# Kernel optimization log

Measured on AMD Instinct MI355X. Metric: run time of the kernel, lower is better.

## Reference

```python
import jax, jax.numpy as jnp
import numpy as np

GROUPS = 16
GROUP_SIZE = 16
K = 3
KK = K * K
BN_EPS = 1e-5


def setup_inputs() -> dict:
    key = jax.random.key(0)
    ks = jax.random.split(key, 6)
    B, C, H, W = 16, 256, 56, 56
    mid = C // 4  # rd_ratio = 4
    x = jax.random.normal(ks[0], (B, C, H, W), dtype=jnp.float32)
    w1 = jax.random.normal(ks[1], (mid, C), dtype=jnp.float32) * (1.0 / np.sqrt(C))
    bn_gamma = jnp.ones((mid,), dtype=jnp.float32)
    bn_beta = jnp.zeros((mid,), dtype=jnp.float32)
    bn_mean = jax.random.normal(ks[2], (mid,), dtype=jnp.float32) * 0.1
    bn_var = jax.random.uniform(ks[3], (mid,), dtype=jnp.float32, minval=0.5, maxval=1.5)
    w2 = jax.random.normal(ks[4], (KK * GROUPS, mid), dtype=jnp.float32) * (1.0 / np.sqrt(mid))
    b2 = jax.random.normal(ks[5], (KK * GROUPS,), dtype=jnp.float32) * 0.01
    return {"x": x, "w1": w1, "bn_gamma": bn_gamma, "bn_beta": bn_beta,
            "bn_mean": bn_mean, "bn_var": bn_var, "w2": w2, "b2": b2}


def reference(x, w1, bn_gamma, bn_beta, bn_mean, bn_var, w2, b2):
    B, C, H, W = x.shape
    # conv1: 1x1 conv + BatchNorm (eval) + ReLU
    t = jnp.einsum('bchw,oc->bohw', x, w1)
    scale = bn_gamma / jnp.sqrt(bn_var + BN_EPS)
    t = t * scale[None, :, None, None] + (bn_beta - bn_mean * scale)[None, :, None, None]
    t = jax.nn.relu(t)
    # conv2: 1x1 conv producing per-pixel kernels (B, KK*groups, H, W)
    weight = jnp.einsum('bchw,oc->bohw', t, w2) + b2[None, :, None, None]
    weight = weight.reshape(B, GROUPS, 1, KK, H, W)
    # unfold: extract 3x3 patches (pad=1, stride=1), kernel positions row-major
    xp = jnp.pad(x, ((0, 0), (0, 0), (1, 1), (1, 1)))
    patches = jnp.stack(
        [xp[:, :, i:i + H, j:j + W] for i in range(K) for j in range(K)],
        axis=2)  # (B, C, KK, H, W), matches torch unfold's (c*KK + kk) layout
    patches = patches.reshape(B, GROUPS, GROUP_SIZE, KK, H, W)
    out = (weight * patches).sum(axis=3).reshape(B, C, H, W)
    return out
```

## Files before the change

### kernel.cpp

```cpp
#include <hip/hip_runtime.h>


#define Cn    256
#define MID   64
#define Hn    56
#define Wn    56
#define HW    3136
#define Bn    16
#define NPIX  (Bn * HW)
#define CHW   (Cn * HW)
#define NKK   9
#define NG    16
#define GSZ   16
#define PXT   64
#define BN_EPS 1e-5f

#define GLOAD_LDS(src, dst, sz)                                                        \
  __builtin_amdgcn_global_load_lds(                                                    \
      (const __attribute__((address_space(1))) void*)(src),                            \
      (__attribute__((address_space(3))) void*)(dst), (sz), 0, 0)

__global__ __launch_bounds__(256) void prep_kernel(
    const float* __restrict__ w1,
    const float* __restrict__ gamma,
    const float* __restrict__ beta,
    const float* __restrict__ mean,
    const float* __restrict__ var,
    float* __restrict__ w1f,
    float* __restrict__ bias1) {
  int idx = blockIdx.x * 256 + threadIdx.x;
  if (idx < MID * Cn) {
    int c = idx >> 6;
    int o = idx & 63;
    float scale = gamma[o] / sqrtf(var[o] + BN_EPS);
    w1f[idx] = w1[o * Cn + c] * scale;
  } else if (idx < MID * Cn + MID) {
    int o = idx - MID * Cn;
    float scale = gamma[o] / sqrtf(var[o] + BN_EPS);
    bias1[o] = beta[o] - mean[o] * scale;
  }
}

__global__ __launch_bounds__(256) void conv1_kernel(
    const float* __restrict__ x,
    const float* __restrict__ w1f,
    const float* __restrict__ bias1,
    float* __restrict__ t) {
  __shared__ __align__(16) float sb[4096];

  const int tid = threadIdx.x;
  const int px  = tid & 63;
  const int wvv = tid >> 6;
  const int wv  = __builtin_amdgcn_readfirstlane(wvv);

  const int px0 = blockIdx.x * PXT;
  const int b   = px0 / HW;
  const int hw0 = px0 - b * HW;
  const float* xb = x + (size_t)b * CHW + hw0;

#pragma unroll
  for (int j = 0; j < 4; ++j) {
    const int c = (wv << 2) + j;
    GLOAD_LDS(xb + (size_t)c * HW + px, &sb[c * 64], 4);
  }
  GLOAD_LDS(w1f + (wv << 8) + (px << 2), &sb[2048 + (wv << 8)], 16);
  __syncthreads();

  float acc[16];
#pragma unroll
  for (int j = 0; j < 16; ++j) acc[j] = 0.0f;

  for (int k = 0; k < 16; ++k) {
    const int cur = k & 1;
    if (k < 15) {
      const int nb = cur ^ 1;
      const int kb = k + 1;
#pragma unroll
      for (int j = 0; j < 4; ++j) {
        const int c = (wv << 2) + j;
        GLOAD_LDS(xb + (size_t)(kb * 16 + c) * HW + px, &sb[nb * 1024 + c * 64], 4);
      }
      GLOAD_LDS(w1f + kb * 1024 + (wv << 8) + (px << 2),
                &sb[2048 + nb * 1024 + (wv << 8)], 16);
    }
    const float* lx = &sb[cur * 1024];
    const float* lw = &sb[2048 + cur * 1024 + (wv << 4)];
#pragma unroll
    for (int c = 0; c < 16; ++c) {
      const float xv = lx[(c << 6) + px];
      const float4 w40 = *(const float4*)(lw + (c << 6) + 0);
      const float4 w41 = *(const float4*)(lw + (c << 6) + 4);
      const float4 w42 = *(const float4*)(lw + (c << 6) + 8);
      const float4 w43 = *(const float4*)(lw + (c << 6) + 12);
      acc[0]  = fmaf(xv, w40.x, acc[0]);
      acc[1]  = fmaf(xv, w40.y, acc[1]);
      acc[2]  = fmaf(xv, w40.z, acc[2]);
      acc[3]  = fmaf(xv, w40.w, acc[3]);
      acc[4]  = fmaf(xv, w41.x, acc[4]);
      acc[5]  = fmaf(xv, w41.y, acc[5]);
      acc[6]  = fmaf(xv, w41.z, acc[6]);
      acc[7]  = fmaf(xv, w41.w, acc[7]);
      acc[8]  = fmaf(xv, w42.x, acc[8]);
      acc[9]  = fmaf(xv, w42.y, acc[9]);
      acc[10] = fmaf(xv, w42.z, acc[10]);
      acc[11] = fmaf(xv, w42.w, acc[11]);
      acc[12] = fmaf(xv, w43.x, acc[12]);
      acc[13] = fmaf(xv, w43.y, acc[13]);
      acc[14] = fmaf(xv, w43.z, acc[14]);
      acc[15] = fmaf(xv, w43.w, acc[15]);
    }
    __syncthreads();
  }

#pragma unroll
  for (int j = 0; j < 16; ++j) {
    const int o = (wv << 4) + j;
    t[(size_t)o * NPIX + px0 + px] = fmaxf(acc[j] + bias1[o], 0.0f);
  }
}

__global__ __launch_bounds__(256) void conv2_inv_kernel(
    const float* __restrict__ x,
    const float* __restrict__ t,
    const float* __restrict__ w2,
    const float* __restrict__ b2,
    float* __restrict__ out) {
  __shared__ float lt[MID][PXT];
  __shared__ __align__(16) float lw2f[4 * NKK * MID];

  const int tid = threadIdx.x;
  const int px  = tid & 63;
  const int wvv = tid >> 6;
  const int wv  = __builtin_amdgcn_readfirstlane(wvv);

  const int bid = blockIdx.x;
  const int pc  = bid >> 2;
  const int gq  = bid & 3;
  const int g   = (gq << 2) + wv;

  const int px0 = pc * PXT;
  const int b   = px0 / HW;
  const int hw0 = px0 - b * HW;

#pragma unroll
  for (int j = 0; j < 16; ++j) {
    const int o = (wv << 4) + j;
    GLOAD_LDS(t + (size_t)o * NPIX + px0 + px, &lt[o][0], 4);
  }
  for (int ch = wv; ch < 9; ch += 4) {
    GLOAD_LDS(w2 + (size_t)gq * (4 * NKK * MID) + (ch << 8) + (px << 2),
              &lw2f[ch << 8], 16);
  }
  __syncthreads();

  float a[NKK];
#pragma unroll
  for (int kk = 0; kk < NKK; ++kk) a[kk] = b2[g * NKK + kk];
  const float* wq = &lw2f[wv * (NKK * MID)];
#pragma unroll 4
  for (int o4 = 0; o4 < MID; o4 += 4) {
    const float t0 = lt[o4 + 0][px];
    const float t1 = lt[o4 + 1][px];
    const float t2 = lt[o4 + 2][px];
    const float t3 = lt[o4 + 3][px];
#pragma unroll
    for (int kk = 0; kk < NKK; ++kk) {
      const float4 w4 = *(const float4*)&wq[(kk << 6) + o4];
      a[kk] = fmaf(t3, w4.w, fmaf(t2, w4.z, fmaf(t1, w4.y, fmaf(t0, w4.x, a[kk]))));
    }
  }

  const int hw = hw0 + px;
  const int h  = hw / Wn;
  const int w  = hw - h * Wn;

  int off[NKK];
  unsigned vmask = 0;
#pragma unroll
  for (int kk = 0; kk < NKK; ++kk) {
    const int di  = kk / 3 - 1;
    const int dj  = kk % 3 - 1;
    const int h2  = h + di;
    const int w2v = w + dj;
    const bool valid = ((unsigned)h2 < (unsigned)Hn) && ((unsigned)w2v < (unsigned)Wn);
    off[kk] = valid ? (h2 * Wn + w2v) : hw;
    vmask |= (valid ? 1u : 0u) << kk;
  }

  float wk[NKK];
#pragma unroll
  for (int kk = 0; kk < NKK; ++kk)
    wk[kk] = ((vmask >> kk) & 1u) ? a[kk] : 0.0f;

  const float* xc = x + (size_t)b * CHW + (size_t)(g * GSZ) * HW;
  float* ob = out + (size_t)b * CHW + (size_t)(g * GSZ) * HW + hw;
#pragma unroll 4
  for (int cc = 0; cc < GSZ; ++cc) {
    const float* xp = xc + (size_t)cc * HW;
    float s0 = wk[0] * xp[off[0]];
    float s1 = wk[1] * xp[off[1]];
    float s2 = wk[2] * xp[off[2]];
    s0 = fmaf(wk[3], xp[off[3]], s0);
    s1 = fmaf(wk[4], xp[off[4]], s1);
    s2 = fmaf(wk[5], xp[off[5]], s2);
    s0 = fmaf(wk[6], xp[off[6]], s0);
    s1 = fmaf(wk[7], xp[off[7]], s1);
    s2 = fmaf(wk[8], xp[off[8]], s2);
    ob[(size_t)cc * HW] = s0 + s1 + s2;
  }
}

extern "C" void kernel_launch(void* const* d_in, const int* in_sizes, int n_in,
                              void* d_out, int out_size, void* d_ws, size_t ws_size,
                              hipStream_t stream) {
  const float* x     = (const float*)d_in[0];
  const float* w1    = (const float*)d_in[1];
  const float* gamma = (const float*)d_in[2];
  const float* beta  = (const float*)d_in[3];
  const float* mean  = (const float*)d_in[4];
  const float* var   = (const float*)d_in[5];
  const float* w2    = (const float*)d_in[6];
  const float* b2    = (const float*)d_in[7];
  float* out = (float*)d_out;

  char* ws = (char*)d_ws;
  float* t     = (float*)ws;
  float* w1f   = (float*)(ws + (size_t)MID * NPIX * 4);
  float* bias1 = (float*)(ws + (size_t)MID * NPIX * 4 + (size_t)MID * Cn * 4);

  prep_kernel<<<(MID * Cn + MID + 255) / 256, 256, 0, stream>>>(
      w1, gamma, beta, mean, var, w1f, bias1);
  conv1_kernel<<<NPIX / PXT, 256, 0, stream>>>(x, w1f, bias1, t);
  conv2_inv_kernel<<<NPIX / PXT * 4, 256, 0, stream>>>(x, t, w2, b2, out);
}
```

Baseline: 176.4 us.

## Split conv1 output channels across two blocks and read weights from global memory

conv1 now launches twice as many blocks, each computing 32 of the 64 output channels with 8 accumulators per thread. Weights are read directly from global memory through wave-uniform addresses instead of being staged in LDS. Both kernels now use 16-byte global-to-LDS loads for the activation tiles. The aim is more parallelism, lower register and LDS pressure, and fewer load instructions. The cost is that x is read twice in conv1 and weight loads go through the cache rather than LDS.

Measured after the change: 161.9 us. -8.2%, faster.

```diff
diff --git a/kernel.cpp b/kernel.cpp
--- a/kernel.cpp
+++ b/kernel.cpp
@@ -46,75 +46,57 @@
     const float* __restrict__ w1f,
     const float* __restrict__ bias1,
     float* __restrict__ t) {
-  __shared__ __align__(16) float sb[4096];
+  __shared__ __align__(16) float lx[2][16][PXT];
 
   const int tid = threadIdx.x;
   const int px  = tid & 63;
-  const int wvv = tid >> 6;
-  const int wv  = __builtin_amdgcn_readfirstlane(wvv);
-
-  const int px0 = blockIdx.x * PXT;
+  const int wv  = __builtin_amdgcn_readfirstlane(tid >> 6);
+
+  const int bid = blockIdx.x;
+  const int pc  = bid >> 1;
+  const int oh  = bid & 1;
+  const int px0 = pc * PXT;
   const int b   = px0 / HW;
   const int hw0 = px0 - b * HW;
   const float* xb = x + (size_t)b * CHW + hw0;
 
-#pragma unroll
-  for (int j = 0; j < 4; ++j) {
-    const int c = (wv << 2) + j;
-    GLOAD_LDS(xb + (size_t)c * HW + px, &sb[c * 64], 4);
-  }
-  GLOAD_LDS(w1f + (wv << 8) + (px << 2), &sb[2048 + (wv << 8)], 16);
+  const int rsub = px >> 4;
+  const int csub = (px & 15) << 2;
+
+  GLOAD_LDS(xb + (size_t)((wv << 2) + rsub) * HW + csub, &lx[0][wv << 2][0], 16);
   __syncthreads();
 
-  float acc[16];
-#pragma unroll
-  for (int j = 0; j < 16; ++j) acc[j] = 0.0f;
+  float acc[8];
+#pragma unroll
+  for (int j = 0; j < 8; ++j) acc[j] = 0.0f;
 
   for (int k = 0; k < 16; ++k) {
     const int cur = k & 1;
     if (k < 15) {
-      const int nb = cur ^ 1;
-      const int kb = k + 1;
-#pragma unroll
-      for (int j = 0; j < 4; ++j) {
-        const int c = (wv << 2) + j;
-        GLOAD_LDS(xb + (size_t)(kb * 16 + c) * HW + px, &sb[nb * 1024 + c * 64], 4);
-      }
-      GLOAD_LDS(w1f + kb * 1024 + (wv << 8) + (px << 2),
-                &sb[2048 + nb * 1024 + (wv << 8)], 16);
+      GLOAD_LDS(xb + (size_t)((k + 1) * 16 + (wv << 2) + rsub) * HW + csub,
+                &lx[cur ^ 1][wv << 2][0], 16);
     }
-    const float* lx = &sb[cur * 1024];
-    const float* lw = &sb[2048 + cur * 1024 + (wv << 4)];
 #pragma unroll
     for (int c = 0; c < 16; ++c) {
-      const float xv = lx[(c << 6) + px];
-      const float4 w40 = *(const float4*)(lw + (c << 6) + 0);
-      const float4 w41 = *(const float4*)(lw + (c << 6) + 4);
-      const float4 w42 = *(const float4*)(lw + (c << 6) + 8);
-      const float4 w43 = *(const float4*)(lw + (c << 6) + 12);
-      acc[0]  = fmaf(xv, w40.x, acc[0]);
-      acc[1]  = fmaf(xv, w40.y, acc[1]);
-      acc[2]  = fmaf(xv, w40.z, acc[2]);
-      acc[3]  = fmaf(xv, w40.w, acc[3]);
-      acc[4]  = fmaf(xv, w41.x, acc[4]);
-      acc[5]  = fmaf(xv, w41.y, acc[5]);
-      acc[6]  = fmaf(xv, w41.z, acc[6]);
-      acc[7]  = fmaf(xv, w41.w, acc[7]);
-      acc[8]  = fmaf(xv, w42.x, acc[8]);
-      acc[9]  = fmaf(xv, w42.y, acc[9]);
-      acc[10] = fmaf(xv, w42.z, acc[10]);
-      acc[11] = fmaf(xv, w42.w, acc[11]);
-      acc[12] = fmaf(xv, w43.x, acc[12]);
-      acc[13] = fmaf(xv, w43.y, acc[13]);
-      acc[14] = fmaf(xv, w43.z, acc[14]);
-      acc[15] = fmaf(xv, w43.w, acc[15]);
+      const float xv = lx[cur][c][px];
+      const float* wr = w1f + (((k << 4) + c) << 6) + (oh << 5) + (wv << 3);
+      const float4 wa = *(const float4*)(wr + 0);
+      const float4 wb = *(const float4*)(wr + 4);
+      acc[0] = fmaf(xv, wa.x, acc[0]);
+      acc[1] = fmaf(xv, wa.y, acc[1]);
+      acc[2] = fmaf(xv, wa.z, acc[2]);
+      acc[3] = fmaf(xv, wa.w, acc[3]);
+      acc[4] = fmaf(xv, wb.x, acc[4]);
+      acc[5] = fmaf(xv, wb.y, acc[5]);
+      acc[6] = fmaf(xv, wb.z, acc[6]);
+      acc[7] = fmaf(xv, wb.w, acc[7]);
     }
     __syncthreads();
   }
 
 #pragma unroll
-  for (int j = 0; j < 16; ++j) {
-    const int o = (wv << 4) + j;
+  for (int j = 0; j < 8; ++j) {
+    const int o = (oh << 5) + (wv << 3) + j;
     t[(size_t)o * NPIX + px0 + px] = fmaxf(acc[j] + bias1[o], 0.0f);
   }
 }
@@ -125,13 +107,11 @@
     const float* __restrict__ w2,
     const float* __restrict__ b2,
     float* __restrict__ out) {
-  __shared__ float lt[MID][PXT];
-  __shared__ __align__(16) float lw2f[4 * NKK * MID];
+  __shared__ __align__(16) float lt[MID][PXT];
 
   const int tid = threadIdx.x;
   const int px  = tid & 63;
-  const int wvv = tid >> 6;
-  const int wv  = __builtin_amdgcn_readfirstlane(wvv);
+  const int wv  = __builtin_amdgcn_readfirstlane(tid >> 6);
 
   const int bid = blockIdx.x;
   const int pc  = bid >> 2;
@@ -142,21 +122,21 @@
   const int b   = px0 / HW;
   const int hw0 = px0 - b * HW;
 
-#pragma unroll
-  for (int j = 0; j < 16; ++j) {
-    const int o = (wv << 4) + j;
-    GLOAD_LDS(t + (size_t)o * NPIX + px0 + px, &lt[o][0], 4);
-  }
-  for (int ch = wv; ch < 9; ch += 4) {
-    GLOAD_LDS(w2 + (size_t)gq * (4 * NKK * MID) + (ch << 8) + (px << 2),
-              &lw2f[ch << 8], 16);
+  const int rsub = px >> 4;
+  const int csub = (px & 15) << 2;
+
+#pragma unroll
+  for (int j = 0; j < 4; ++j) {
+    const int r0 = (wv << 4) + (j << 2);
+    GLOAD_LDS(t + (size_t)(r0 + rsub) * NPIX + px0 + csub, &lt[r0][0], 16);
   }
   __syncthreads();
 
   float a[NKK];
 #pragma unroll
   for (int kk = 0; kk < NKK; ++kk) a[kk] = b2[g * NKK + kk];
-  const float* wq = &lw2f[wv * (NKK * MID)];
+
+  const float* wg = w2 + (size_t)g * (NKK * MID);
 #pragma unroll 4
   for (int o4 = 0; o4 < MID; o4 += 4) {
     const float t0 = lt[o4 + 0][px];
@@ -165,7 +145,7 @@
     const float t3 = lt[o4 + 3][px];
 #pragma unroll
     for (int kk = 0; kk < NKK; ++kk) {
-      const float4 w4 = *(const float4*)&wq[(kk << 6) + o4];
+      const float4 w4 = *(const float4*)(wg + (kk << 6) + o4);
       a[kk] = fmaf(t3, w4.w, fmaf(t2, w4.z, fmaf(t1, w4.y, fmaf(t0, w4.x, a[kk]))));
     }
   }
@@ -230,6 +210,6 @@
 
   prep_kernel<<<(MID * Cn + MID + 255) / 256, 256, 0, stream>>>(
       w1, gamma, beta, mean, var, w1f, bias1);
-  conv1_kernel<<<NPIX / PXT, 256, 0, stream>>>(x, w1f, bias1, t);
+  conv1_kernel<<<NPIX / PXT * 2, 256, 0, stream>>>(x, w1f, bias1, t);
   conv2_inv_kernel<<<NPIX / PXT * 4, 256, 0, stream>>>(x, t, w2, b2, out);
 }
```
